# Performance work log

Hardware: AMD Instinct MI355X
Metric: run time of the kernel (lower is better)

## Reference

```python
import jax, jax.numpy as jnp
import numpy as np

DIM = 1024
HEADS = 16
HD = DIM // HEADS  # 64
EPS = 1.1920928955078125e-07  # torch.finfo(float32).eps, RMSNorm default


def setup_inputs() -> dict:
    key = jax.random.key(0)
    ks = jax.random.split(key, 8)
    s = 0.02
    return {
        "x": jax.random.normal(ks[0], (2, 2048, DIM), jnp.float32),
        "pe": jax.random.normal(ks[1], (1, 1, 2048, HD // 2, 2, 2), jnp.float32),
        "qkv_w": jax.random.normal(ks[2], (3 * DIM, DIM), jnp.float32) * s,
        "qkv_b": jax.random.normal(ks[3], (3 * DIM,), jnp.float32) * s,
        "q_norm_w": jnp.ones((HD,), jnp.float32),
        "k_norm_w": jnp.ones((HD,), jnp.float32),
        "proj_w": jax.random.normal(ks[4], (DIM, DIM), jnp.float32) * s,
        "proj_b": jax.random.normal(ks[5], (DIM,), jnp.float32) * s,
    }


def _rms_norm(t, w):
    var = jnp.mean(jnp.square(t), axis=-1, keepdims=True)
    return t * jax.lax.rsqrt(var + EPS) * w


def _apply_rope(t, pe):
    # t: [B,H,L,D]; pe: [1,1,L,D/2,2,2]
    B, H, L, D = t.shape
    tp = t.reshape(B, H, L, D // 2, 1, 2)
    out = pe[..., 0] * tp[..., 0] + pe[..., 1] * tp[..., 1]  # [B,H,L,D/2,2]
    return out.reshape(B, H, L, D)


def reference(x, pe, qkv_w, qkv_b, q_norm_w, k_norm_w, proj_w, proj_b):
    B, L, _ = x.shape
    qkv = x @ qkv_w.T + qkv_b  # [B,L,3*DIM]
    qkv = qkv.reshape(B, L, 3, HEADS, HD).transpose(2, 0, 3, 1, 4)  # [3,B,H,L,D]
    q, k, v = qkv[0], qkv[1], qkv[2]
    q = _rms_norm(q, q_norm_w)
    k = _rms_norm(k, k_norm_w)
    q = _apply_rope(q, pe)
    k = _apply_rope(k, pe)
    scale = 1.0 / np.sqrt(HD).astype(np.float32)
    scores = jnp.einsum("bhqd,bhkd->bhqk", q, k) * scale  # [B,H,L,L]
    attn = jax.nn.softmax(scores, axis=-1)
    o = jnp.einsum("bhqk,bhkd->bhqd", attn, v)  # [B,H,L,D]
    o = o.transpose(0, 2, 1, 3).reshape(B, L, DIM)  # B L (H D)
    return o @ proj_w.T + proj_b
```

## Files before the change

kernel.cpp:

```cpp
#include <hip/hip_runtime.h>
#include <hip/hip_bf16.h>

#define DIM   1024
#define HEADS 16
#define HD    64
#define BB    2
#define LL    2048
#define MTOT  (BB*LL)
#define EPSV  1.1920928955078125e-07f

typedef __attribute__((ext_vector_type(8))) short bf16x8;
typedef __attribute__((ext_vector_type(4))) float f32x4;
typedef unsigned short ushort_t;

__device__ __forceinline__ float bf2f(ushort_t u) {
    unsigned int x = ((unsigned int)u) << 16;
    return __builtin_bit_cast(float, x);
}
__device__ __forceinline__ ushort_t f2bf(float f) {
    unsigned int x = __builtin_bit_cast(unsigned int, f);
    unsigned int r = (x + 0x7FFFu + ((x >> 16) & 1u)) >> 16;
    return (ushort_t)r;
}
__device__ __forceinline__ unsigned int cvt_pk_bf16(float lo, float hi) {
    unsigned int r;
    asm("v_cvt_pk_bf16_f32 %0, %1, %2" : "=v"(r) : "v"(lo), "v"(hi));
    return r;
}

__global__ __launch_bounds__(256) void cvt_all_k(const float* __restrict__ a, int na,
                                                 const float* __restrict__ b, int nb,
                                                 const float* __restrict__ c,
                                                 ushort_t* __restrict__ oa,
                                                 ushort_t* __restrict__ ob,
                                                 ushort_t* __restrict__ oc) {
    int i = (blockIdx.x * 256 + threadIdx.x) * 4;
    const float* src;
    ushort_t* dst;
    int off;
    if (i < na)            { src = a; dst = oa; off = i; }
    else if (i < na + nb)  { src = b; dst = ob; off = i - na; }
    else                   { src = c; dst = oc; off = i - na - nb; }
    float4 v = *(const float4*)(src + off);
    ushort4 o;
    o.x = f2bf(v.x); o.y = f2bf(v.y); o.z = f2bf(v.z); o.w = f2bf(v.w);
    *(ushort4*)(dst + off) = o;
}

__global__ __launch_bounds__(256, 2) void gemm128(const ushort_t* __restrict__ A,
                                                  const ushort_t* __restrict__ Bt,
                                                  const float* __restrict__ bias,
                                                  ushort_t* __restrict__ C,
                                                  int M, int N, int K) {
    __shared__ __attribute__((aligned(16))) ushort_t Asm[2][128 * 64];
    __shared__ __attribute__((aligned(16))) ushort_t Bsm[2][128 * 64];
    const int tid = threadIdx.x;
    const int lane = tid & 63, wid = tid >> 6;
    const int wm = wid >> 1, wn = wid & 1;
    const int r = lane & 15, g = lane >> 4;
    const int m0 = blockIdx.y * 128, n0 = blockIdx.x * 128;

    int srow[4], sgx[4];
#pragma unroll
    for (int p = 0; p < 4; ++p) {
        int c = p * 256 + tid;
        srow[p] = c >> 3;
        sgx[p] = ((c & 7) ^ (srow[p] & 7)) * 8;
    }
    const ushort_t *pa[4], *pb[4];
#pragma unroll
    for (int p = 0; p < 4; ++p) {
        pa[p] = A + (size_t)(m0 + srow[p]) * K + sgx[p];
        pb[p] = Bt + (size_t)(n0 + srow[p]) * K + sgx[p];
    }

    f32x4 acc[4][4] = {};

    auto stage = [&](int kt, int slot) {
        const int kc = kt * 64;
#pragma unroll
        for (int p = 0; p < 4; ++p) {
            __builtin_amdgcn_global_load_lds(
                (const __attribute__((address_space(1))) void*)(pa[p] + kc),
                (__attribute__((address_space(3))) void*)(&Asm[slot][0] + (p * 256 + wid * 64) * 8), 16, 0, 0);
            __builtin_amdgcn_global_load_lds(
                (const __attribute__((address_space(1))) void*)(pb[p] + kc),
                (__attribute__((address_space(3))) void*)(&Bsm[slot][0] + (p * 256 + wid * 64) * 8), 16, 0, 0);
        }
    };

    stage(0, 0);
    asm volatile("s_waitcnt vmcnt(0)" ::: "memory");
    __builtin_amdgcn_s_barrier();
    asm volatile("" ::: "memory");

    const int nkt = K >> 6;
    for (int kt = 0; kt < nkt; ++kt) {
        const int slot = kt & 1;
        if (kt + 1 < nkt) stage(kt + 1, slot ^ 1);
        const ushort_t* As = &Asm[slot][0];
        const ushort_t* Bs = &Bsm[slot][0];
#pragma unroll
        for (int ks = 0; ks < 2; ++ks) {
            bf16x8 af[4], bf[4];
#pragma unroll
            for (int mi = 0; mi < 4; ++mi) {
                int row = wm * 64 + mi * 16 + r;
                af[mi] = *(const bf16x8*)(As + row * 64 + (((ks * 4 + g) ^ (row & 7)) * 8));
            }
#pragma unroll
            for (int ni = 0; ni < 4; ++ni) {
                int row = wn * 64 + ni * 16 + r;
                bf[ni] = *(const bf16x8*)(Bs + row * 64 + (((ks * 4 + g) ^ (row & 7)) * 8));
            }
            __builtin_amdgcn_s_setprio(1);
#pragma unroll
            for (int mi = 0; mi < 4; ++mi)
#pragma unroll
                for (int ni = 0; ni < 4; ++ni)
                    acc[mi][ni] = __builtin_amdgcn_mfma_f32_16x16x32_bf16(af[mi], bf[ni], acc[mi][ni], 0, 0, 0);
            __builtin_amdgcn_s_setprio(0);
        }
        asm volatile("s_waitcnt vmcnt(0)" ::: "memory");
        __builtin_amdgcn_s_barrier();
        asm volatile("" ::: "memory");
    }

#pragma unroll
    for (int mi = 0; mi < 4; mi++)
#pragma unroll
        for (int ni = 0; ni < 4; ni++) {
            int col = n0 + wn * 64 + ni * 16 + r;
            float bv = bias[col];
#pragma unroll
            for (int reg = 0; reg < 4; reg++) {
                int row = m0 + wm * 64 + mi * 16 + g * 4 + reg;
                C[(size_t)row * N + col] = f2bf(acc[mi][ni][reg] + bv);
            }
        }
}

__global__ __launch_bounds__(256, 2) void gemm_pj(const ushort_t* __restrict__ A,
                                                  const ushort_t* __restrict__ Bt,
                                                  const float* __restrict__ bias,
                                                  float* __restrict__ C,
                                                  int M, int N, int K) {
    __shared__ __attribute__((aligned(16))) ushort_t Asm[2][128 * 64];
    __shared__ __attribute__((aligned(16))) ushort_t Bsm[2][64 * 64];
    const int tid = threadIdx.x;
    const int lane = tid & 63, wid = tid >> 6;
    const int wm = wid >> 1, wn = wid & 1;
    const int r = lane & 15, g = lane >> 4;
    const int m0 = blockIdx.y * 128, n0 = blockIdx.x * 64;

    int srow[4], sgx[4];
#pragma unroll
    for (int p = 0; p < 4; ++p) {
        int c = p * 256 + tid;
        srow[p] = c >> 3;
        sgx[p] = ((c & 7) ^ (srow[p] & 7)) * 8;
    }
    const ushort_t *pa[4], *pb[2];
#pragma unroll
    for (int p = 0; p < 4; ++p) pa[p] = A + (size_t)(m0 + srow[p]) * K + sgx[p];
#pragma unroll
    for (int p = 0; p < 2; ++p) pb[p] = Bt + (size_t)(n0 + srow[p]) * K + sgx[p];

    f32x4 acc[4][2] = {};

    auto stage = [&](int kt, int slot) {
        const int kc = kt * 64;
#pragma unroll
        for (int p = 0; p < 4; ++p)
            __builtin_amdgcn_global_load_lds(
                (const __attribute__((address_space(1))) void*)(pa[p] + kc),
                (__attribute__((address_space(3))) void*)(&Asm[slot][0] + (p * 256 + wid * 64) * 8), 16, 0, 0);
#pragma unroll
        for (int p = 0; p < 2; ++p)
            __builtin_amdgcn_global_load_lds(
                (const __attribute__((address_space(1))) void*)(pb[p] + kc),
                (__attribute__((address_space(3))) void*)(&Bsm[slot][0] + (p * 256 + wid * 64) * 8), 16, 0, 0);
    };

    stage(0, 0);
    asm volatile("s_waitcnt vmcnt(0)" ::: "memory");
    __builtin_amdgcn_s_barrier();
    asm volatile("" ::: "memory");

    const int nkt = K >> 6;
    for (int kt = 0; kt < nkt; ++kt) {
        const int slot = kt & 1;
        if (kt + 1 < nkt) stage(kt + 1, slot ^ 1);
        const ushort_t* As = &Asm[slot][0];
        const ushort_t* Bs = &Bsm[slot][0];
#pragma unroll
        for (int ks = 0; ks < 2; ++ks) {
            bf16x8 af[4], bf[2];
#pragma unroll
            for (int mi = 0; mi < 4; ++mi) {
                int row = wm * 64 + mi * 16 + r;
                af[mi] = *(const bf16x8*)(As + row * 64 + (((ks * 4 + g) ^ (row & 7)) * 8));
            }
#pragma unroll
            for (int ni = 0; ni < 2; ++ni) {
                int row = wn * 32 + ni * 16 + r;
                bf[ni] = *(const bf16x8*)(Bs + row * 64 + (((ks * 4 + g) ^ (row & 7)) * 8));
            }
            __builtin_amdgcn_s_setprio(1);
#pragma unroll
            for (int mi = 0; mi < 4; ++mi)
#pragma unroll
                for (int ni = 0; ni < 2; ++ni)
                    acc[mi][ni] = __builtin_amdgcn_mfma_f32_16x16x32_bf16(af[mi], bf[ni], acc[mi][ni], 0, 0, 0);
            __builtin_amdgcn_s_setprio(0);
        }
        asm volatile("s_waitcnt vmcnt(0)" ::: "memory");
        __builtin_amdgcn_s_barrier();
        asm volatile("" ::: "memory");
    }

#pragma unroll
    for (int mi = 0; mi < 4; mi++)
#pragma unroll
        for (int ni = 0; ni < 2; ni++) {
            int col = n0 + wn * 32 + ni * 16 + r;
            float bv = bias[col];
#pragma unroll
            for (int reg = 0; reg < 4; reg++) {
                int row = m0 + wm * 64 + mi * 16 + g * 4 + reg;
                C[(size_t)row * N + col] = acc[mi][ni][reg] + bv;
            }
        }
}

__global__ __launch_bounds__(256) void norm_rope_k(const ushort_t* __restrict__ qkv,
                                                   const float* __restrict__ pe,
                                                   const float* __restrict__ qnw,
                                                   const float* __restrict__ knw,
                                                   ushort_t* __restrict__ qh,
                                                   ushort_t* __restrict__ kh,
                                                   ushort_t* __restrict__ vT) {
    __shared__ ushort_t T[64][68];
    const int tid = threadIdx.x;
    const int lane = tid & 63, w = tid >> 6;
    const int rg = lane >> 4;
    const int d4 = (lane & 15) * 4;
    const int l0 = blockIdx.x * 64;
    const int t  = blockIdx.y;
    const int bh = blockIdx.z;
    const int b = bh >> 4, h = bh & 15;

    if (t == 2) {
#pragma unroll
        for (int i = 0; i < 4; ++i) {
            int ll = w * 16 + rg + 4 * i;
            int m = b * 2048 + l0 + ll;
            ushort4 v = *(const ushort4*)(qkv + (size_t)m * 3072 + 2048 + h * 64 + d4);
            *(ushort4*)(&T[ll][d4]) = v;
        }
        __syncthreads();
        const int d = tid >> 2, lq = (tid & 3) * 16;
        ushort_t* dst = vT + ((size_t)(bh * 64 + d)) * 2048 + l0 + lq;
#pragma unroll
        for (int c = 0; c < 4; ++c) {
            ushort4 o;
            o.x = T[lq + c * 4 + 0][d];
            o.y = T[lq + c * 4 + 1][d];
            o.z = T[lq + c * 4 + 2][d];
            o.w = T[lq + c * 4 + 3][d];
            *(ushort4*)(dst + c * 4) = o;
        }
        return;
    }

    const float* nwp = (t == 0) ? qnw : knw;
    const float4 nwv = *(const float4*)(nwp + d4);
    ushort_t* dst = (t == 0) ? qh : kh;
    const float qscale = (t == 0) ? 0.125f : 1.0f;
#pragma unroll
    for (int i = 0; i < 4; ++i) {
        int ll = w * 16 + rg + 4 * i;
        int l = l0 + ll;
        int m = b * 2048 + l;
        ushort4 vv = *(const ushort4*)(qkv + (size_t)m * 3072 + t * 1024 + h * 64 + d4);
        float v0 = bf2f(vv.x), v1 = bf2f(vv.y), v2 = bf2f(vv.z), v3 = bf2f(vv.w);
        float ss = v0 * v0 + v1 * v1 + v2 * v2 + v3 * v3;
        ss += __shfl_xor(ss, 1, 64);
        ss += __shfl_xor(ss, 2, 64);
        ss += __shfl_xor(ss, 4, 64);
        ss += __shfl_xor(ss, 8, 64);
        float rms = rsqrtf(ss * (1.0f / 64.0f) + EPSV);
        v0 *= rms * nwv.x; v1 *= rms * nwv.y; v2 *= rms * nwv.z; v3 *= rms * nwv.w;
        float4 p0 = *(const float4*)(pe + (size_t)l * 128 + 2 * d4);
        float4 p1 = *(const float4*)(pe + (size_t)l * 128 + 2 * d4 + 4);
        float o0 = (p0.x * v0 + p0.y * v1) * qscale;
        float o1 = (p0.z * v0 + p0.w * v1) * qscale;
        float o2 = (p1.x * v2 + p1.y * v3) * qscale;
        float o3 = (p1.z * v2 + p1.w * v3) * qscale;
        ushort4 o;
        o.x = f2bf(o0); o.y = f2bf(o1); o.z = f2bf(o2); o.w = f2bf(o3);
        *(ushort4*)(dst + ((size_t)bh * 2048 + l) * 64 + d4) = o;
    }
}

__global__ __launch_bounds__(256, 2) void attn_k(const ushort_t* __restrict__ qh,
                                                 const ushort_t* __restrict__ kh,
                                                 const ushort_t* __restrict__ vT,
                                                 ushort_t* __restrict__ ob) {
    __shared__ __attribute__((aligned(16))) ushort_t Ksm[2][64 * 64];
    __shared__ __attribute__((aligned(16))) ushort_t Vsm[2][64 * 64];
    __shared__ __attribute__((aligned(16))) ushort_t Plds[4][2][16 * 64];

    const int tid = threadIdx.x;
    const int lane = tid & 63, wid = tid >> 6;
    const int r = lane & 15, g = lane >> 4;
    const int qt = blockIdx.x, bh = blockIdx.y;
    const int q0 = qt * 128 + wid * 32;
    const ushort_t* Q  = qh + (size_t)bh * LL * 64;
    const ushort_t* Kb = kh + (size_t)bh * LL * 64;
    const ushort_t* Vt = vT + (size_t)bh * 64 * LL;

    int row_[2], ccx_[2];
#pragma unroll
    for (int q = 0; q < 2; ++q) {
        int c = q * 256 + tid;
        row_[q] = c >> 3;
        ccx_[q] = (c & 7) ^ (row_[q] & 7);
    }
    const int swz = (r & 7) * 8;

    bf16x8 qf[2][2];
#pragma unroll
    for (int mf = 0; mf < 2; ++mf)
#pragma unroll
        for (int hf = 0; hf < 2; ++hf)
            qf[mf][hf] = *(const bf16x8*)(Q + (size_t)(q0 + mf * 16 + r) * 64 + hf * 32 + g * 8);

    f32x4 acc[2][4] = {};
    float mrow[2] = {-1e30f, -1e30f};
    float srow[2] = {0.f, 0.f};
    const f32x4 zero = {};

#pragma unroll
    for (int q = 0; q < 2; ++q) {
        __builtin_amdgcn_global_load_lds(
            (const __attribute__((address_space(1))) void*)(Kb + (size_t)row_[q] * 64 + ccx_[q] * 8),
            (__attribute__((address_space(3))) void*)(&Ksm[0][0] + (q * 256 + wid * 64) * 8), 16, 0, 0);
        __builtin_amdgcn_global_load_lds(
            (const __attribute__((address_space(1))) void*)(Vt + (size_t)row_[q] * 2048 + ccx_[q] * 8),
            (__attribute__((address_space(3))) void*)(&Vsm[0][0] + (q * 256 + wid * 64) * 8), 16, 0, 0);
    }
    __syncthreads();

    int buf = 0;
    for (int it = 0; it < 32; ++it) {
        if (it < 31) {
            int kvn = (it + 1) * 64;
#pragma unroll
            for (int q = 0; q < 2; ++q) {
                __builtin_amdgcn_global_load_lds(
                    (const __attribute__((address_space(1))) void*)(Kb + (size_t)(kvn + row_[q]) * 64 + ccx_[q] * 8),
                    (__attribute__((address_space(3))) void*)(&Ksm[buf ^ 1][0] + (q * 256 + wid * 64) * 8), 16, 0, 0);
                __builtin_amdgcn_global_load_lds(
                    (const __attribute__((address_space(1))) void*)(Vt + (size_t)row_[q] * 2048 + kvn + ccx_[q] * 8),
                    (__attribute__((address_space(3))) void*)(&Vsm[buf ^ 1][0] + (q * 256 + wid * 64) * 8), 16, 0, 0);
            }
        }
        const ushort_t* Kl = &Ksm[buf][0];
        const ushort_t* Vl = &Vsm[buf][0];

        bf16x8 kf[4][2];
#pragma unroll
        for (int kt = 0; kt < 4; ++kt)
#pragma unroll
            for (int hf = 0; hf < 2; ++hf)
                kf[kt][hf] = *(const bf16x8*)(Kl + (kt * 16 + r) * 64 + (((hf * 4 + g) * 8) ^ swz));

        f32x4 s[2][4];
        __builtin_amdgcn_s_setprio(1);
#pragma unroll
        for (int mf = 0; mf < 2; ++mf)
#pragma unroll
            for (int kt = 0; kt < 4; ++kt) {
                f32x4 t0 = __builtin_amdgcn_mfma_f32_16x16x32_bf16(kf[kt][0], qf[mf][0], zero, 0, 0, 0);
                s[mf][kt] = __builtin_amdgcn_mfma_f32_16x16x32_bf16(kf[kt][1], qf[mf][1], t0, 0, 0, 0);
            }
        __builtin_amdgcn_s_setprio(0);

#pragma unroll
        for (int mf = 0; mf < 2; ++mf) {
            float pm = -1e30f;
#pragma unroll
            for (int kt = 0; kt < 4; ++kt)
#pragma unroll
                for (int reg = 0; reg < 4; ++reg) pm = fmaxf(pm, s[mf][kt][reg]);
            pm = fmaxf(pm, __shfl_xor(pm, 16, 64));
            pm = fmaxf(pm, __shfl_xor(pm, 32, 64));
            bool skip = (__all(pm <= mrow[mf] + 8.0f) != 0);
            float mn, al;
            if (skip) {
                mn = mrow[mf];
            } else {
                mn = fmaxf(mrow[mf], pm);
                al = __expf(mrow[mf] - mn);
                mrow[mf] = mn;
            }
            float rs = 0.f;
#pragma unroll
            for (int kt = 0; kt < 4; ++kt)
#pragma unroll
                for (int reg = 0; reg < 4; ++reg) {
                    float p = __expf(s[mf][kt][reg] - mn);
                    s[mf][kt][reg] = p;
                    rs += p;
                }
            rs += __shfl_xor(rs, 16, 64);
            rs += __shfl_xor(rs, 32, 64);
            if (skip) {
                srow[mf] += rs;
            } else {
                srow[mf] = srow[mf] * al + rs;
                float ab[4];
#pragma unroll
                for (int reg = 0; reg < 4; ++reg) ab[reg] = __shfl(al, g * 4 + reg, 16);
#pragma unroll
                for (int dt = 0; dt < 4; ++dt)
#pragma unroll
                    for (int reg = 0; reg < 4; ++reg) acc[mf][dt][reg] *= ab[reg];
            }
#pragma unroll
            for (int kt = 0; kt < 4; ++kt) {
                uint2 pw;
                pw.x = cvt_pk_bf16(s[mf][kt][0], s[mf][kt][1]);
                pw.y = cvt_pk_bf16(s[mf][kt][2], s[mf][kt][3]);
                *(uint2*)((ushort_t*)&Plds[wid][mf][0] + r * 64 + (((2 * kt + (g >> 1)) * 8) ^ swz) + (g & 1) * 4) = pw;
            }
        }
        asm volatile("s_waitcnt lgkmcnt(0)" ::: "memory");
        __builtin_amdgcn_sched_barrier(0);

        bf16x8 pa[2][2];
#pragma unroll
        for (int mf = 0; mf < 2; ++mf)
#pragma unroll
            for (int hf = 0; hf < 2; ++hf)
                pa[mf][hf] = *(const bf16x8*)(&Plds[wid][mf][0] + r * 64 + (((hf * 4 + g) * 8) ^ swz));

        __builtin_amdgcn_s_setprio(1);
#pragma unroll
        for (int dt = 0; dt < 4; ++dt)
#pragma unroll
            for (int hv = 0; hv < 2; ++hv) {
                bf16x8 vf = *(const bf16x8*)(Vl + (dt * 16 + r) * 64 + (((hv * 4 + g) * 8) ^ swz));
#pragma unroll
                for (int mf = 0; mf < 2; ++mf)
                    acc[mf][dt] = __builtin_amdgcn_mfma_f32_16x16x32_bf16(pa[mf][hv], vf, acc[mf][dt], 0, 0, 0);
            }
        __builtin_amdgcn_s_setprio(0);

        __syncthreads();
        buf ^= 1;
    }

    int b = bh >> 4, h = bh & 15;
#pragma unroll
    for (int mf = 0; mf < 2; ++mf) {
        float sinv = 1.0f / srow[mf];
        float sb[4];
#pragma unroll
        for (int reg = 0; reg < 4; ++reg) sb[reg] = __shfl(sinv, g * 4 + reg, 16);
#pragma unroll
        for (int dt = 0; dt < 4; ++dt)
#pragma unroll
            for (int reg = 0; reg < 4; ++reg) {
                int l = q0 + mf * 16 + g * 4 + reg;
                ob[((size_t)(b * 2048 + l)) * 1024 + h * 64 + dt * 16 + r] =
                    f2bf(acc[mf][dt][reg] * sb[reg]);
            }
    }
}

extern "C" void kernel_launch(void* const* d_in, const int* in_sizes, int n_in,
                              void* d_out, int out_size, void* d_ws, size_t ws_size,
                              hipStream_t stream) {
    const float* x      = (const float*)d_in[0];
    const float* pe     = (const float*)d_in[1];
    const float* qkv_w  = (const float*)d_in[2];
    const float* qkv_b  = (const float*)d_in[3];
    const float* qnw    = (const float*)d_in[4];
    const float* knw    = (const float*)d_in[5];
    const float* proj_w = (const float*)d_in[6];
    const float* proj_b = (const float*)d_in[7];
    float* out = (float*)d_out;

    char* ws = (char*)d_ws;
    ushort_t* xb    = (ushort_t*)(ws);
    ushort_t* wqkv  = (ushort_t*)(ws + 8388608);
    ushort_t* wproj = (ushort_t*)(ws + 8388608 + 6291456);
    ushort_t* qkvb  = (ushort_t*)(ws + 16777216);
    ushort_t* qhp   = (ushort_t*)(ws + 16777216 + 25165824);
    ushort_t* khp   = (ushort_t*)(ws + 16777216 + 25165824 + 8388608);
    ushort_t* vtp   = (ushort_t*)(ws + 16777216 + 25165824 + 2 * 8388608);
    ushort_t* obp   = qkvb;

    const int na = MTOT * DIM, nb = 3 * DIM * DIM, nc = DIM * DIM;
    cvt_all_k<<<(na + nb + nc) / 1024, 256, 0, stream>>>(x, na, qkv_w, nb, proj_w,
                                                         xb, wqkv, wproj);

    gemm128<<<dim3(3 * DIM / 128, MTOT / 128), 256, 0, stream>>>(xb, wqkv, qkv_b, qkvb,
                                                                 MTOT, 3 * DIM, DIM);
    norm_rope_k<<<dim3(32, 3, 32), 256, 0, stream>>>(qkvb, pe, qnw, knw, qhp, khp, vtp);
    attn_k<<<dim3(16, 32), 256, 0, stream>>>(qhp, khp, vtp, obp);
    gemm_pj<<<dim3(DIM / 64, MTOT / 128), 256, 0, stream>>>(obp, wproj, proj_b, out,
                                                            MTOT, DIM, DIM);
}
```

Baseline: 217.6 us.

## Fuse RMSNorm, RoPE and V transpose into QKV GEMM epilogue; use exp2 softmax

```diff
diff --git a/kernel.cpp b/kernel.cpp
--- a/kernel.cpp
+++ b/kernel.cpp
@@ -8,6 +8,8 @@
 #define LL    2048
 #define MTOT  (BB*LL)
 #define EPSV  1.1920928955078125e-07f
+#define QSCALE 0.18033688011112042f
+#define THR2   11.541560327111707f
 
 typedef __attribute__((ext_vector_type(8))) short bf16x8;
 typedef __attribute__((ext_vector_type(4))) float f32x4;
@@ -25,6 +27,11 @@
 __device__ __forceinline__ unsigned int cvt_pk_bf16(float lo, float hi) {
     unsigned int r;
     asm("v_cvt_pk_bf16_f32 %0, %1, %2" : "=v"(r) : "v"(lo), "v"(hi));
+    return r;
+}
+__device__ __forceinline__ float exp2_fast(float x) {
+    float r;
+    asm("v_exp_f32 %0, %1" : "=v"(r) : "v"(x));
     return r;
 }
 
@@ -47,13 +54,17 @@
     *(ushort4*)(dst + off) = o;
 }
 
-__global__ __launch_bounds__(256, 2) void gemm128(const ushort_t* __restrict__ A,
-                                                  const ushort_t* __restrict__ Bt,
-                                                  const float* __restrict__ bias,
-                                                  ushort_t* __restrict__ C,
-                                                  int M, int N, int K) {
-    __shared__ __attribute__((aligned(16))) ushort_t Asm[2][128 * 64];
-    __shared__ __attribute__((aligned(16))) ushort_t Bsm[2][128 * 64];
+__global__ __launch_bounds__(256, 2) void gemm_qkv_fused(const ushort_t* __restrict__ A,
+                                                         const ushort_t* __restrict__ Bt,
+                                                         const float* __restrict__ bias,
+                                                         const float* __restrict__ pe,
+                                                         const float* __restrict__ qnw,
+                                                         const float* __restrict__ knw,
+                                                         ushort_t* __restrict__ qh,
+                                                         ushort_t* __restrict__ kh,
+                                                         ushort_t* __restrict__ vT) {
+    __shared__ __attribute__((aligned(16))) ushort_t smem[32768];
+    const int K = 1024;
     const int tid = threadIdx.x;
     const int lane = tid & 63, wid = tid >> 6;
     const int wm = wid >> 1, wn = wid & 1;
@@ -82,10 +93,10 @@
         for (int p = 0; p < 4; ++p) {
             __builtin_amdgcn_global_load_lds(
                 (const __attribute__((address_space(1))) void*)(pa[p] + kc),
-                (__attribute__((address_space(3))) void*)(&Asm[slot][0] + (p * 256 + wid * 64) * 8), 16, 0, 0);
+                (__attribute__((address_space(3))) void*)(smem + slot * 8192 + (p * 256 + wid * 64) * 8), 16, 0, 0);
             __builtin_amdgcn_global_load_lds(
                 (const __attribute__((address_space(1))) void*)(pb[p] + kc),
-                (__attribute__((address_space(3))) void*)(&Bsm[slot][0] + (p * 256 + wid * 64) * 8), 16, 0, 0);
+                (__attribute__((address_space(3))) void*)(smem + 16384 + slot * 8192 + (p * 256 + wid * 64) * 8), 16, 0, 0);
         }
     };
 
@@ -94,12 +105,11 @@
     __builtin_amdgcn_s_barrier();
     asm volatile("" ::: "memory");
 
-    const int nkt = K >> 6;
-    for (int kt = 0; kt < nkt; ++kt) {
+    for (int kt = 0; kt < 16; ++kt) {
         const int slot = kt & 1;
-        if (kt + 1 < nkt) stage(kt + 1, slot ^ 1);
-        const ushort_t* As = &Asm[slot][0];
-        const ushort_t* Bs = &Bsm[slot][0];
+        if (kt + 1 < 16) stage(kt + 1, slot ^ 1);
+        const ushort_t* As = smem + slot * 8192;
+        const ushort_t* Bs = smem + 16384 + slot * 8192;
 #pragma unroll
         for (int ks = 0; ks < 2; ++ks) {
             bf16x8 af[4], bf[4];
@@ -126,18 +136,82 @@
         asm volatile("" ::: "memory");
     }
 
-#pragma unroll
-    for (int mi = 0; mi < 4; mi++)
-#pragma unroll
-        for (int ni = 0; ni < 4; ni++) {
-            int col = n0 + wn * 64 + ni * 16 + r;
-            float bv = bias[col];
-#pragma unroll
-            for (int reg = 0; reg < 4; reg++) {
-                int row = m0 + wm * 64 + mi * 16 + g * 4 + reg;
-                C[(size_t)row * N + col] = f2bf(acc[mi][ni][reg] + bv);
-            }
-        }
+    const int t = n0 >> 10;
+    const int h = ((n0 & 1023) >> 6) + wn;
+    const int b = m0 >> 11;
+    const int bh = b * 16 + h;
+    const int l0 = (m0 & 2047) + wm * 64;
+
+    float bv[4];
+#pragma unroll
+    for (int ni = 0; ni < 4; ++ni) bv[ni] = bias[n0 + wn * 64 + ni * 16 + r];
+#pragma unroll
+    for (int mi = 0; mi < 4; ++mi)
+#pragma unroll
+        for (int ni = 0; ni < 4; ++ni)
+#pragma unroll
+            for (int reg = 0; reg < 4; ++reg) acc[mi][ni][reg] += bv[ni];
+
+    if (t < 2) {
+        const float* nw = (t == 0) ? qnw : knw;
+        float nwv[4];
+#pragma unroll
+        for (int ni = 0; ni < 4; ++ni) nwv[ni] = nw[ni * 16 + r];
+        const float qsc = (t == 0) ? QSCALE : 1.0f;
+        ushort_t* dst = ((t == 0) ? qh : kh) + (size_t)bh * 2048 * 64;
+#pragma unroll
+        for (int mi = 0; mi < 4; ++mi)
+#pragma unroll
+            for (int reg = 0; reg < 4; ++reg) {
+                float ss = 0.f;
+#pragma unroll
+                for (int ni = 0; ni < 4; ++ni) {
+                    float xv = acc[mi][ni][reg];
+                    ss = fmaf(xv, xv, ss);
+                }
+                ss += __shfl_xor(ss, 1, 64);
+                ss += __shfl_xor(ss, 2, 64);
+                ss += __shfl_xor(ss, 4, 64);
+                ss += __shfl_xor(ss, 8, 64);
+                float rms = rsqrtf(ss * (1.0f / 64.0f) + EPSV);
+                int l = l0 + mi * 16 + g * 4 + reg;
+                const float* per = pe + (size_t)l * 128 + 2 * r;
+#pragma unroll
+                for (int ni = 0; ni < 4; ++ni) {
+                    float nv = acc[mi][ni][reg] * rms * nwv[ni];
+                    float partner = __shfl_xor(nv, 1, 64);
+                    float2 pv = *(const float2*)(per + ni * 32);
+                    float e0 = (r & 1) ? partner : nv;
+                    float e1 = (r & 1) ? nv : partner;
+                    dst[(size_t)l * 64 + ni * 16 + r] = f2bf((pv.x * e0 + pv.y * e1) * qsc);
+                }
+            }
+    } else {
+        ushort_t* T = smem + wid * 4352;
+#pragma unroll
+        for (int mi = 0; mi < 4; ++mi)
+#pragma unroll
+            for (int ni = 0; ni < 4; ++ni)
+#pragma unroll
+                for (int reg = 0; reg < 4; ++reg)
+                    T[(mi * 16 + g * 4 + reg) * 66 + ni * 16 + r] = f2bf(acc[mi][ni][reg]);
+        asm volatile("s_waitcnt lgkmcnt(0)" ::: "memory");
+        const int dd = lane >> 2, lq = (lane & 3) * 16;
+#pragma unroll
+        for (int pass = 0; pass < 4; ++pass) {
+            int d = pass * 16 + dd;
+            ushort_t* dst = vT + ((size_t)(bh * 64 + d)) * 2048 + (m0 & 2047) + wm * 64 + lq;
+#pragma unroll
+            for (int c = 0; c < 4; ++c) {
+                ushort4 o;
+                o.x = T[(lq + c * 4 + 0) * 66 + d];
+                o.y = T[(lq + c * 4 + 1) * 66 + d];
+                o.z = T[(lq + c * 4 + 2) * 66 + d];
+                o.w = T[(lq + c * 4 + 3) * 66 + d];
+                *(ushort4*)(dst + c * 4) = o;
+            }
+        }
+    }
 }
 
 __global__ __launch_bounds__(256, 2) void gemm_pj(const ushort_t* __restrict__ A,
@@ -224,83 +298,13 @@
 #pragma unroll
         for (int ni = 0; ni < 2; ni++) {
             int col = n0 + wn * 32 + ni * 16 + r;
-            float bv = bias[col];
+            float bvv = bias[col];
 #pragma unroll
             for (int reg = 0; reg < 4; reg++) {
                 int row = m0 + wm * 64 + mi * 16 + g * 4 + reg;
-                C[(size_t)row * N + col] = acc[mi][ni][reg] + bv;
-            }
-        }
-}
-
-__global__ __launch_bounds__(256) void norm_rope_k(const ushort_t* __restrict__ qkv,
-                                                   const float* __restrict__ pe,
-                                                   const float* __restrict__ qnw,
-                                                   const float* __restrict__ knw,
-                                                   ushort_t* __restrict__ qh,
-                                                   ushort_t* __restrict__ kh,
-                                                   ushort_t* __restrict__ vT) {
-    __shared__ ushort_t T[64][68];
-    const int tid = threadIdx.x;
-    const int lane = tid & 63, w = tid >> 6;
-    const int rg = lane >> 4;
-    const int d4 = (lane & 15) * 4;
-    const int l0 = blockIdx.x * 64;
-    const int t  = blockIdx.y;
-    const int bh = blockIdx.z;
-    const int b = bh >> 4, h = bh & 15;
-
-    if (t == 2) {
-#pragma unroll
-        for (int i = 0; i < 4; ++i) {
-            int ll = w * 16 + rg + 4 * i;
-            int m = b * 2048 + l0 + ll;
-            ushort4 v = *(const ushort4*)(qkv + (size_t)m * 3072 + 2048 + h * 64 + d4);
-            *(ushort4*)(&T[ll][d4]) = v;
-        }
-        __syncthreads();
-        const int d = tid >> 2, lq = (tid & 3) * 16;
-        ushort_t* dst = vT + ((size_t)(bh * 64 + d)) * 2048 + l0 + lq;
-#pragma unroll
-        for (int c = 0; c < 4; ++c) {
-            ushort4 o;
-            o.x = T[lq + c * 4 + 0][d];
-            o.y = T[lq + c * 4 + 1][d];
-            o.z = T[lq + c * 4 + 2][d];
-            o.w = T[lq + c * 4 + 3][d];
-            *(ushort4*)(dst + c * 4) = o;
-        }
-        return;
-    }
-
-    const float* nwp = (t == 0) ? qnw : knw;
-    const float4 nwv = *(const float4*)(nwp + d4);
-    ushort_t* dst = (t == 0) ? qh : kh;
-    const float qscale = (t == 0) ? 0.125f : 1.0f;
-#pragma unroll
-    for (int i = 0; i < 4; ++i) {
-        int ll = w * 16 + rg + 4 * i;
-        int l = l0 + ll;
-        int m = b * 2048 + l;
-        ushort4 vv = *(const ushort4*)(qkv + (size_t)m * 3072 + t * 1024 + h * 64 + d4);
-        float v0 = bf2f(vv.x), v1 = bf2f(vv.y), v2 = bf2f(vv.z), v3 = bf2f(vv.w);
-        float ss = v0 * v0 + v1 * v1 + v2 * v2 + v3 * v3;
-        ss += __shfl_xor(ss, 1, 64);
-        ss += __shfl_xor(ss, 2, 64);
-        ss += __shfl_xor(ss, 4, 64);
-        ss += __shfl_xor(ss, 8, 64);
-        float rms = rsqrtf(ss * (1.0f / 64.0f) + EPSV);
-        v0 *= rms * nwv.x; v1 *= rms * nwv.y; v2 *= rms * nwv.z; v3 *= rms * nwv.w;
-        float4 p0 = *(const float4*)(pe + (size_t)l * 128 + 2 * d4);
-        float4 p1 = *(const float4*)(pe + (size_t)l * 128 + 2 * d4 + 4);
-        float o0 = (p0.x * v0 + p0.y * v1) * qscale;
-        float o1 = (p0.z * v0 + p0.w * v1) * qscale;
-        float o2 = (p1.x * v2 + p1.y * v3) * qscale;
-        float o3 = (p1.z * v2 + p1.w * v3) * qscale;
-        ushort4 o;
-        o.x = f2bf(o0); o.y = f2bf(o1); o.z = f2bf(o2); o.w = f2bf(o3);
-        *(ushort4*)(dst + ((size_t)bh * 2048 + l) * 64 + d4) = o;
-    }
+                C[(size_t)row * N + col] = acc[mi][ni][reg] + bvv;
+            }
+        }
 }
 
 __global__ __launch_bounds__(256, 2) void attn_k(const ushort_t* __restrict__ qh,
@@ -396,13 +400,13 @@
                 for (int reg = 0; reg < 4; ++reg) pm = fmaxf(pm, s[mf][kt][reg]);
             pm = fmaxf(pm, __shfl_xor(pm, 16, 64));
             pm = fmaxf(pm, __shfl_xor(pm, 32, 64));
-            bool skip = (__all(pm <= mrow[mf] + 8.0f) != 0);
+            bool skip = (__all(pm <= mrow[mf] + THR2) != 0);
             float mn, al;
             if (skip) {
                 mn = mrow[mf];
             } else {
                 mn = fmaxf(mrow[mf], pm);
-                al = __expf(mrow[mf] - mn);
+                al = exp2_fast(mrow[mf] - mn);
                 mrow[mf] = mn;
             }
             float rs = 0.f;
@@ -410,7 +414,7 @@
             for (int kt = 0; kt < 4; ++kt)
 #pragma unroll
                 for (int reg = 0; reg < 4; ++reg) {
-                    float p = __expf(s[mf][kt][reg] - mn);
+                    float p = exp2_fast(s[mf][kt][reg] - mn);
                     s[mf][kt][reg] = p;
                     rs += p;
                 }
@@ -497,19 +501,17 @@
     ushort_t* xb    = (ushort_t*)(ws);
     ushort_t* wqkv  = (ushort_t*)(ws + 8388608);
     ushort_t* wproj = (ushort_t*)(ws + 8388608 + 6291456);
-    ushort_t* qkvb  = (ushort_t*)(ws + 16777216);
+    ushort_t* obp   = (ushort_t*)(ws + 16777216);
     ushort_t* qhp   = (ushort_t*)(ws + 16777216 + 25165824);
     ushort_t* khp   = (ushort_t*)(ws + 16777216 + 25165824 + 8388608);
     ushort_t* vtp   = (ushort_t*)(ws + 16777216 + 25165824 + 2 * 8388608);
-    ushort_t* obp   = qkvb;
 
     const int na = MTOT * DIM, nb = 3 * DIM * DIM, nc = DIM * DIM;
     cvt_all_k<<<(na + nb + nc) / 1024, 256, 0, stream>>>(x, na, qkv_w, nb, proj_w,
                                                          xb, wqkv, wproj);
 
-    gemm128<<<dim3(3 * DIM / 128, MTOT / 128), 256, 0, stream>>>(xb, wqkv, qkv_b, qkvb,
-                                                                 MTOT, 3 * DIM, DIM);
-    norm_rope_k<<<dim3(32, 3, 32), 256, 0, stream>>>(qkvb, pe, qnw, knw, qhp, khp, vtp);
+    gemm_qkv_fused<<<dim3(24, 32), 256, 0, stream>>>(xb, wqkv, qkv_b, pe, qnw, knw,
+                                                     qhp, khp, vtp);
     attn_k<<<dim3(16, 32), 256, 0, stream>>>(qhp, khp, vtp, obp);
     gemm_pj<<<dim3(DIM / 64, MTOT / 128), 256, 0, stream>>>(obp, wproj, proj_b, out,
                                                             MTOT, DIM, DIM);
```

Result: faster. 211.3 us (-2.9%).
